# Optimization experiments

Measured on AMD Instinct MI355X. Metric: run time of the kernel, lower is better.

The kernel has to match this reference:

```python
import jax, jax.numpy as jnp
import numpy as np

B, TQ, TP, D = 4, 512, 512, 256


def setup_inputs() -> dict:
    key = jax.random.key(0)
    ks = jax.random.split(key, 5)
    return {
        "q": jax.random.normal(ks[0], (B, TQ, D), dtype=jnp.float32),
        "p": jax.random.normal(ks[1], (B, TP, D), dtype=jnp.float32),
        "W0": jax.random.normal(ks[2], (D, D), dtype=jnp.float32) / np.sqrt(D),
        "W1": jax.random.normal(ks[3], (D, D), dtype=jnp.float32) / np.sqrt(D),
        "vc": jax.random.normal(ks[4], (D, 1), dtype=jnp.float32) * 0.05,
    }


def reference(q, p, W0, W1, vc):
    # q: [B,Tq,Dq], p: [B,Tp,Dp]
    prod_q = jnp.einsum('bqd,de->bqe', q, W0)   # [B,Tq,dim]
    prod_p = jnp.einsum('bpd,de->bpe', p, W1)   # [B,Tp,dim]
    # additive attention energies: tanh over broadcast sum [B,Tp,Tq,dim]
    energy = jnp.tanh(prod_p[:, :, None, :] + prod_q[:, None, :, :])
    scores = jnp.einsum('bpqe,e->bpq', energy, vc[:, 0])  # [B,Tp,Tq]
    # original softmax is over axis=-2 of [B,Tp,Tq], i.e. the Tp axis
    weights = jax.nn.softmax(scores, axis=1)   # [B,Tp,Tq]
    # weighted sum over the Tq axis of (tiled) q
    attention_q = jnp.einsum('bpq,bqd->bpd', weights, q)  # [B,Tp,Dq]
    return attention_q
```

## Files before the change

### kernel.cpp

```cpp
#include <hip/hip_runtime.h>

#define NB 4
#define TT 512
#define DD 256
#define K2L2E    2.885390081777927f
#define NEG2L2E (-2.885390081777927f)

#if defined(__has_builtin)
# if __has_builtin(__builtin_amdgcn_global_load_lds)
#  define HAS_GLL 1
# endif
#endif

__device__ __forceinline__ void stage16(const float* __restrict__ g, float* l) {
#ifdef HAS_GLL
    __builtin_amdgcn_global_load_lds((const __attribute__((address_space(1))) void*)g,
                                     (__attribute__((address_space(3))) void*)l, 16, 0, 0);
#else
    *(float4*)l = *(const float4*)g;
#endif
}

__global__ __launch_bounds__(256) void proj_exp_kernel(
    const float* __restrict__ qin, const float* __restrict__ pin,
    const float* __restrict__ W0, const float* __restrict__ W1,
    float* __restrict__ expQ, float* __restrict__ expP)
{
    const int blk = blockIdx.x;
    const int wh = blk >> 8, tid = blk & 255;
    const int m0 = (tid >> 2) * 32, n0 = (tid & 3) * 64;
    const float* A = wh ? pin : qin;
    const float* W = wh ? W1 : W0;
    float* OUT     = wh ? expP : expQ;

    __shared__ __align__(16) float As[32 * 34];
    __shared__ __align__(16) float Bs[32 * 64];

    const int t  = threadIdx.x;
    const int ar = t >> 3, ac4 = (t & 7) * 4;
    const int br = t >> 4, bc4 = (t & 15) * 4;
    const int tn = t >> 4, tm = t & 15;

    const float* Ap = A + (long)(m0 + ar) * DD + ac4;

    float4 av  = *(const float4*)Ap;
    float4 bv0 = *(const float4*)(W + (long)br * DD + n0 + bc4);
    float4 bv1 = *(const float4*)(W + (long)(br + 16) * DD + n0 + bc4);

    float acc[2][4] = {};

    for (int c = 0; c < 8; ++c) {
        As[(ac4 + 0) * 34 + ar] = av.x;
        As[(ac4 + 1) * 34 + ar] = av.y;
        As[(ac4 + 2) * 34 + ar] = av.z;
        As[(ac4 + 3) * 34 + ar] = av.w;
        *(float4*)&Bs[br * 64 + bc4]        = bv0;
        *(float4*)&Bs[(br + 16) * 64 + bc4] = bv1;
        __syncthreads();
        if (c < 7) {
            int k1 = (c + 1) * 32;
            av  = *(const float4*)(Ap + k1);
            bv0 = *(const float4*)(W + (long)(k1 + br) * DD + n0 + bc4);
            bv1 = *(const float4*)(W + (long)(k1 + 16 + br) * DD + n0 + bc4);
        }
        #pragma unroll
        for (int kk = 0; kk < 32; ++kk) {
            float2 a = *(const float2*)&As[kk * 34 + 2 * tm];
            float4 b = *(const float4*)&Bs[kk * 64 + 4 * tn];
            float aa[2] = {a.x, a.y};
            float bb[4] = {b.x, b.y, b.z, b.w};
            #pragma unroll
            for (int i = 0; i < 2; ++i)
                #pragma unroll
                for (int j = 0; j < 4; ++j)
                    acc[i][j] = __builtin_fmaf(aa[i], bb[j], acc[i][j]);
        }
        __syncthreads();
    }

    const int  bi = m0 >> 9;
    const int  ml = (m0 & 511) + 2 * tm;
    #pragma unroll
    for (int j = 0; j < 4; ++j) {
        int d = n0 + 4 * tn + j;
        float2 st;
        st.x = __builtin_amdgcn_exp2f(acc[0][j] * K2L2E);
        st.y = __builtin_amdgcn_exp2f(acc[1][j] * K2L2E);
        *(float2*)(OUT + ((long)bi * DD + d) * TT + ml) = st;
    }
}

__global__ __launch_bounds__(512, 4) void score_kernel(
    const float* __restrict__ expP, const float* __restrict__ expQ,
    const float* __restrict__ vc, float* __restrict__ ebuf, float* __restrict__ lpart)
{
    const int b = blockIdx.z, pt = blockIdx.y, qt = blockIdx.x;
    const int p0 = pt * 32, q0 = qt * 64;
    const int t  = threadIdx.x;
    const int qx = t & 31, py = t >> 5;

    __shared__ __align__(16) float PA[2][64 * 32];
    __shared__ __align__(16) float QB[2][64 * 64];
    __shared__ float vcs[DD];

    const float* gP = expP + (long)b * DD * TT + p0;
    const float* gQ = expQ + (long)b * DD * TT + q0;

    {
        int d = t >> 3, off = (t & 7) * 4;
        stage16(gP + (long)d * TT + off, &PA[0][t * 4]);
    }
    #pragma unroll
    for (int s = 0; s < 2; ++s) {
        int f = t + 512 * s, d = f >> 4, off = (f & 15) * 4;
        stage16(gQ + (long)d * TT + off, &QB[0][f * 4]);
    }
    if (t < DD) vcs[t] = vc[t];
    __syncthreads();

    float acc[2][2] = {};

    for (int c = 0; c < 4; ++c) {
        if (c < 3) {
            int dc = (c + 1) * 64, nb = (c + 1) & 1;
            {
                int d = t >> 3, off = (t & 7) * 4;
                stage16(gP + (long)(dc + d) * TT + off, &PA[nb][t * 4]);
            }
            #pragma unroll
            for (int s = 0; s < 2; ++s) {
                int f = t + 512 * s, d = f >> 4, off = (f & 15) * 4;
                stage16(gQ + (long)(dc + d) * TT + off, &QB[nb][f * 4]);
            }
        }
        const float* PAc = PA[c & 1];
        const float* QBc = QB[c & 1];
        const float* vcb = &vcs[c * 64];
        #pragma unroll 8
        for (int dp = 0; dp < 32; ++dp) {
            float2 vp = *(const float2*)&vcb[2 * dp];
            float vs = vp.x + vp.y;
            float2 A0 = *(const float2*)&PAc[(2 * dp) * 32 + 2 * py];
            float2 A1 = *(const float2*)&PAc[(2 * dp + 1) * 32 + 2 * py];
            float2 B0 = *(const float2*)&QBc[(2 * dp) * 64 + 2 * qx];
            float2 B1 = *(const float2*)&QBc[(2 * dp + 1) * 64 + 2 * qx];
            float a0[2] = {A0.x, A0.y}, a1[2] = {A1.x, A1.y};
            float b0[2] = {B0.x, B0.y}, b1[2] = {B1.x, B1.y};
            #pragma unroll
            for (int i = 0; i < 2; ++i)
                #pragma unroll
                for (int j = 0; j < 2; ++j) {
                    float E0  = a0[i] * b0[j];
                    float E1  = a1[i] * b1[j];
                    float u   = 1.0f + (E0 + E1);
                    float den = __builtin_fmaf(E0, E1, u);
                    float num = __builtin_fmaf(vp.y, E0, __builtin_fmaf(vp.x, E1, vs));
                    acc[i][j] = __builtin_fmaf(num, __builtin_amdgcn_rcpf(den), acc[i][j]);
                }
        }
        __syncthreads();
    }

    float* eb = ebuf + ((long)b * TT + p0) * TT + q0;
    float colp[2] = {0.f, 0.f};
    #pragma unroll
    for (int i = 0; i < 2; ++i) {
        float2 ev;
        ev.x = __builtin_amdgcn_exp2f(acc[i][0] * NEG2L2E);
        ev.y = __builtin_amdgcn_exp2f(acc[i][1] * NEG2L2E);
        *(float2*)(eb + (long)(2 * py + i) * TT + 2 * qx) = ev;
        colp[0] += ev.x; colp[1] += ev.y;
    }
    float* scr = (float*)&PA[0][0];
    *(float2*)&scr[py * 64 + 2 * qx] = make_float2(colp[0], colp[1]);
    __syncthreads();
    if (t < 64) {
        float s = 0.f;
        #pragma unroll
        for (int r = 0; r < 16; ++r) s += scr[r * 64 + t];
        lpart[((long)b * 16 + pt) * TT + q0 + t] = s;
    }
}

__global__ __launch_bounds__(256) void out_kernel(
    const float* __restrict__ ebuf, const float* __restrict__ qin,
    const float* __restrict__ lpart, float* __restrict__ out)
{
    const int b = blockIdx.z, mt = blockIdx.y, nt = blockIdx.x;
    const int m0 = mt * 32, n0 = nt * 32;
    const int t  = threadIdx.x;
    const int tm = t >> 4, tn = t & 15;

    __shared__ __align__(16) float As[64 * 34];
    __shared__ __align__(16) float Bs[64 * 36];
    __shared__ float linv[TT];

    #pragma unroll
    for (int s = 0; s < 2; ++s) {
        int qq = t + 256 * s;
        float sum = 0.f;
        #pragma unroll
        for (int pb = 0; pb < 16; ++pb) sum += lpart[((long)b * 16 + pb) * TT + qq];
        linv[qq] = __builtin_amdgcn_rcpf(sum);
    }
    __syncthreads();

    const float* Ab = ebuf + ((long)b * TT + m0) * TT;
    const float* Bb = qin + (long)b * TT * DD + n0;

    const int ara = t >> 4, aca = (t & 15) * 4;
    const int brb = t >> 3, bcb = (t & 7) * 4;

    float4 av0 = *(const float4*)(Ab + (long)ara * TT + aca);
    float4 av1 = *(const float4*)(Ab + (long)(ara + 16) * TT + aca);
    float4 bv0 = *(const float4*)(Bb + (long)brb * DD + bcb);
    float4 bv1 = *(const float4*)(Bb + (long)(brb + 32) * DD + bcb);

    float acc[2][2] = {};

    for (int c = 0; c < 8; ++c) {
        const int k0 = c * 64;
        As[(aca + 0) * 34 + ara] = av0.x;
        As[(aca + 1) * 34 + ara] = av0.y;
        As[(aca + 2) * 34 + ara] = av0.z;
        As[(aca + 3) * 34 + ara] = av0.w;
        As[(aca + 0) * 34 + ara + 16] = av1.x;
        As[(aca + 1) * 34 + ara + 16] = av1.y;
        As[(aca + 2) * 34 + ara + 16] = av1.z;
        As[(aca + 3) * 34 + ara + 16] = av1.w;
        {
            float s0 = linv[k0 + brb], s1 = linv[k0 + brb + 32];
            float4 w0, w1;
            w0.x = bv0.x * s0; w0.y = bv0.y * s0; w0.z = bv0.z * s0; w0.w = bv0.w * s0;
            w1.x = bv1.x * s1; w1.y = bv1.y * s1; w1.z = bv1.z * s1; w1.w = bv1.w * s1;
            *(float4*)&Bs[brb * 36 + bcb]        = w0;
            *(float4*)&Bs[(brb + 32) * 36 + bcb] = w1;
        }
        __syncthreads();
        if (c < 7) {
            int k1 = (c + 1) * 64;
            av0 = *(const float4*)(Ab + (long)ara * TT + k1 + aca);
            av1 = *(const float4*)(Ab + (long)(ara + 16) * TT + k1 + aca);
            bv0 = *(const float4*)(Bb + (long)(k1 + brb) * DD + bcb);
            bv1 = *(const float4*)(Bb + (long)(k1 + brb + 32) * DD + bcb);
        }
        #pragma unroll
        for (int kk = 0; kk < 64; ++kk) {
            float2 a = *(const float2*)&As[kk * 34 + 2 * tm];
            float2 bb = *(const float2*)&Bs[kk * 36 + 2 * tn];
            acc[0][0] = __builtin_fmaf(a.x, bb.x, acc[0][0]);
            acc[0][1] = __builtin_fmaf(a.x, bb.y, acc[0][1]);
            acc[1][0] = __builtin_fmaf(a.y, bb.x, acc[1][0]);
            acc[1][1] = __builtin_fmaf(a.y, bb.y, acc[1][1]);
        }
        __syncthreads();
    }

    #pragma unroll
    for (int i = 0; i < 2; ++i) {
        float2 v = make_float2(acc[i][0], acc[i][1]);
        *(float2*)(out + ((long)b * TT + m0 + 2 * tm + i) * DD + n0 + 2 * tn) = v;
    }
}

extern "C" void kernel_launch(void* const* d_in, const int* in_sizes, int n_in,
                              void* d_out, int out_size, void* d_ws, size_t ws_size,
                              hipStream_t stream) {
    const float* q  = (const float*)d_in[0];
    const float* p  = (const float*)d_in[1];
    const float* W0 = (const float*)d_in[2];
    const float* W1 = (const float*)d_in[3];
    const float* vc = (const float*)d_in[4];
    float* out = (float*)d_out;

    float* ws    = (float*)d_ws;
    float* expQ  = ws;
    float* expP  = ws + 524288;
    float* ebuf  = ws + 1048576;
    float* lpart = ws + 2097152;

    proj_exp_kernel<<<dim3(512), 256, 0, stream>>>(q, p, W0, W1, expQ, expP);
    score_kernel<<<dim3(8, 16, NB), 512, 0, stream>>>(expP, expQ, vc, ebuf, lpart);
    out_kernel<<<dim3(8, 16, NB), 256, 0, stream>>>(ebuf, q, lpart, out);
}
```

Measured before the change: 128.5 us.

## Use packed FP32 FMA in score loop and retile output GEMM to 4x2

Rewrites the score kernel's inner tanh-identity math on two-wide float vectors so the compiler can emit packed FP32 instructions (v_pk_fma/v_pk_mul), roughly halving VALU issue for that hot loop. The output GEMM is retiled to 128 threads, each computing a 4x2 register tile with packed FMAs, which changes the staging pattern and the LDS padding. This raises per-thread work and register use and halves threads per block, which lowers occupancy in the out kernel.

```diff
diff --git a/kernel.cpp b/kernel.cpp
--- a/kernel.cpp
+++ b/kernel.cpp
@@ -11,6 +11,21 @@
 #  define HAS_GLL 1
 # endif
 #endif
+
+typedef float v2f __attribute__((ext_vector_type(2)));
+
+__device__ __forceinline__ v2f pk_fma(v2f a, v2f b, v2f c) {
+#if defined(__has_builtin)
+# if __has_builtin(__builtin_elementwise_fma)
+    return __builtin_elementwise_fma(a, b, c);
+# else
+    v2f r; r.x = __builtin_fmaf(a.x, b.x, c.x); r.y = __builtin_fmaf(a.y, b.y, c.y); return r;
+# endif
+#else
+    v2f r; r.x = __builtin_fmaf(a.x, b.x, c.x); r.y = __builtin_fmaf(a.y, b.y, c.y); return r;
+#endif
+}
+__device__ __forceinline__ v2f splat2(float s) { v2f r; r.x = s; r.y = s; return r; }
 
 __device__ __forceinline__ void stage16(const float* __restrict__ g, float* l) {
 #ifdef HAS_GLL
@@ -118,7 +133,7 @@
     if (t < DD) vcs[t] = vc[t];
     __syncthreads();
 
-    float acc[2][2] = {};
+    v2f acc[2]; acc[0] = splat2(0.f); acc[1] = splat2(0.f);
 
     for (int c = 0; c < 4; ++c) {
         if (c < 3) {
@@ -139,40 +154,41 @@
         #pragma unroll 8
         for (int dp = 0; dp < 32; ++dp) {
             float2 vp = *(const float2*)&vcb[2 * dp];
-            float vs = vp.x + vp.y;
+            v2f vsv = splat2(vp.x + vp.y);
+            v2f vx  = splat2(vp.x), vy = splat2(vp.y);
             float2 A0 = *(const float2*)&PAc[(2 * dp) * 32 + 2 * py];
             float2 A1 = *(const float2*)&PAc[(2 * dp + 1) * 32 + 2 * py];
-            float2 B0 = *(const float2*)&QBc[(2 * dp) * 64 + 2 * qx];
-            float2 B1 = *(const float2*)&QBc[(2 * dp + 1) * 64 + 2 * qx];
+            v2f B0 = *(const v2f*)&QBc[(2 * dp) * 64 + 2 * qx];
+            v2f B1 = *(const v2f*)&QBc[(2 * dp + 1) * 64 + 2 * qx];
             float a0[2] = {A0.x, A0.y}, a1[2] = {A1.x, A1.y};
-            float b0[2] = {B0.x, B0.y}, b1[2] = {B1.x, B1.y};
             #pragma unroll
-            for (int i = 0; i < 2; ++i)
-                #pragma unroll
-                for (int j = 0; j < 2; ++j) {
-                    float E0  = a0[i] * b0[j];
-                    float E1  = a1[i] * b1[j];
-                    float u   = 1.0f + (E0 + E1);
-                    float den = __builtin_fmaf(E0, E1, u);
-                    float num = __builtin_fmaf(vp.y, E0, __builtin_fmaf(vp.x, E1, vs));
-                    acc[i][j] = __builtin_fmaf(num, __builtin_amdgcn_rcpf(den), acc[i][j]);
-                }
+            for (int i = 0; i < 2; ++i) {
+                v2f E0  = splat2(a0[i]) * B0;
+                v2f E1  = splat2(a1[i]) * B1;
+                v2f u   = (E0 + E1) + 1.0f;
+                v2f den = pk_fma(E0, E1, u);
+                v2f num = pk_fma(vy, E0, pk_fma(vx, E1, vsv));
+                v2f r;
+                r.x = __builtin_amdgcn_rcpf(den.x);
+                r.y = __builtin_amdgcn_rcpf(den.y);
+                acc[i] = pk_fma(num, r, acc[i]);
+            }
         }
         __syncthreads();
     }
 
     float* eb = ebuf + ((long)b * TT + p0) * TT + q0;
-    float colp[2] = {0.f, 0.f};
+    v2f colp = splat2(0.f);
     #pragma unroll
     for (int i = 0; i < 2; ++i) {
         float2 ev;
-        ev.x = __builtin_amdgcn_exp2f(acc[i][0] * NEG2L2E);
-        ev.y = __builtin_amdgcn_exp2f(acc[i][1] * NEG2L2E);
+        ev.x = __builtin_amdgcn_exp2f(acc[i].x * NEG2L2E);
+        ev.y = __builtin_amdgcn_exp2f(acc[i].y * NEG2L2E);
         *(float2*)(eb + (long)(2 * py + i) * TT + 2 * qx) = ev;
-        colp[0] += ev.x; colp[1] += ev.y;
+        colp.x += ev.x; colp.y += ev.y;
     }
     float* scr = (float*)&PA[0][0];
-    *(float2*)&scr[py * 64 + 2 * qx] = make_float2(colp[0], colp[1]);
+    *(float2*)&scr[py * 64 + 2 * qx] = make_float2(colp.x, colp.y);
     __syncthreads();
     if (t < 64) {
         float s = 0.f;
@@ -182,22 +198,23 @@
     }
 }
 
-__global__ __launch_bounds__(256) void out_kernel(
+__global__ __launch_bounds__(128) void out_kernel(
     const float* __restrict__ ebuf, const float* __restrict__ qin,
     const float* __restrict__ lpart, float* __restrict__ out)
 {
-    const int b = blockIdx.z, mt = blockIdx.y, nt = blockIdx.x;
-    const int m0 = mt * 32, n0 = nt * 32;
+    const int b = blockIdx.z, pt = blockIdx.y, dt = blockIdx.x;
+    const int m0 = pt * 32, n0 = dt * 32;
     const int t  = threadIdx.x;
-    const int tm = t >> 4, tn = t & 15;
-
-    __shared__ __align__(16) float As[64 * 34];
+    const int tm = t >> 4;
+    const int tn = t & 15;
+
+    __shared__ __align__(16) float As[64 * 36];
     __shared__ __align__(16) float Bs[64 * 36];
     __shared__ float linv[TT];
 
     #pragma unroll
-    for (int s = 0; s < 2; ++s) {
-        int qq = t + 256 * s;
+    for (int s = 0; s < 4; ++s) {
+        int qq = t + 128 * s;
         float sum = 0.f;
         #pragma unroll
         for (int pb = 0; pb < 16; ++pb) sum += lpart[((long)b * 16 + pb) * TT + qq];
@@ -208,58 +225,60 @@
     const float* Ab = ebuf + ((long)b * TT + m0) * TT;
     const float* Bb = qin + (long)b * TT * DD + n0;
 
-    const int ara = t >> 4, aca = (t & 15) * 4;
-    const int brb = t >> 3, bcb = (t & 7) * 4;
-
-    float4 av0 = *(const float4*)(Ab + (long)ara * TT + aca);
-    float4 av1 = *(const float4*)(Ab + (long)(ara + 16) * TT + aca);
-    float4 bv0 = *(const float4*)(Bb + (long)brb * DD + bcb);
-    float4 bv1 = *(const float4*)(Bb + (long)(brb + 32) * DD + bcb);
-
-    float acc[2][2] = {};
+    const int ar  = t >> 2;
+    const int akc = (t & 3) * 4;
+    const int brr = t >> 3;
+    const int bc4 = (t & 7) * 4;
+
+    float4 av[4], bv[4];
+    #pragma unroll
+    for (int u = 0; u < 4; ++u) {
+        av[u] = *(const float4*)(Ab + (long)ar * TT + 16 * u + akc);
+        bv[u] = *(const float4*)(Bb + (long)(brr + 16 * u) * DD + bc4);
+    }
+
+    v2f acc[4]; acc[0] = splat2(0.f); acc[1] = splat2(0.f);
+    acc[2] = splat2(0.f); acc[3] = splat2(0.f);
 
     for (int c = 0; c < 8; ++c) {
         const int k0 = c * 64;
-        As[(aca + 0) * 34 + ara] = av0.x;
-        As[(aca + 1) * 34 + ara] = av0.y;
-        As[(aca + 2) * 34 + ara] = av0.z;
-        As[(aca + 3) * 34 + ara] = av0.w;
-        As[(aca + 0) * 34 + ara + 16] = av1.x;
-        As[(aca + 1) * 34 + ara + 16] = av1.y;
-        As[(aca + 2) * 34 + ara + 16] = av1.z;
-        As[(aca + 3) * 34 + ara + 16] = av1.w;
-        {
-            float s0 = linv[k0 + brb], s1 = linv[k0 + brb + 32];
-            float4 w0, w1;
-            w0.x = bv0.x * s0; w0.y = bv0.y * s0; w0.z = bv0.z * s0; w0.w = bv0.w * s0;
-            w1.x = bv1.x * s1; w1.y = bv1.y * s1; w1.z = bv1.z * s1; w1.w = bv1.w * s1;
-            *(float4*)&Bs[brb * 36 + bcb]        = w0;
-            *(float4*)&Bs[(brb + 32) * 36 + bcb] = w1;
+        #pragma unroll
+        for (int u = 0; u < 4; ++u) {
+            int kl = 16 * u + akc;
+            As[(kl + 0) * 36 + ar] = av[u].x;
+            As[(kl + 1) * 36 + ar] = av[u].y;
+            As[(kl + 2) * 36 + ar] = av[u].z;
+            As[(kl + 3) * 36 + ar] = av[u].w;
+            float s = linv[k0 + brr + 16 * u];
+            float4 w;
+            w.x = bv[u].x * s; w.y = bv[u].y * s; w.z = bv[u].z * s; w.w = bv[u].w * s;
+            *(float4*)&Bs[(brr + 16 * u) * 36 + bc4] = w;
         }
         __syncthreads();
         if (c < 7) {
             int k1 = (c + 1) * 64;
-            av0 = *(const float4*)(Ab + (long)ara * TT + k1 + aca);
-            av1 = *(const float4*)(Ab + (long)(ara + 16) * TT + k1 + aca);
-            bv0 = *(const float4*)(Bb + (long)(k1 + brb) * DD + bcb);
-            bv1 = *(const float4*)(Bb + (long)(k1 + brb + 32) * DD + bcb);
+            #pragma unroll
+            for (int u = 0; u < 4; ++u) {
+                av[u] = *(const float4*)(Ab + (long)ar * TT + k1 + 16 * u + akc);
+                bv[u] = *(const float4*)(Bb + (long)(k1 + brr + 16 * u) * DD + bc4);
+            }
         }
         #pragma unroll
         for (int kk = 0; kk < 64; ++kk) {
-            float2 a = *(const float2*)&As[kk * 34 + 2 * tm];
-            float2 bb = *(const float2*)&Bs[kk * 36 + 2 * tn];
-            acc[0][0] = __builtin_fmaf(a.x, bb.x, acc[0][0]);
-            acc[0][1] = __builtin_fmaf(a.x, bb.y, acc[0][1]);
-            acc[1][0] = __builtin_fmaf(a.y, bb.x, acc[1][0]);
-            acc[1][1] = __builtin_fmaf(a.y, bb.y, acc[1][1]);
-        }
-        __syncthreads();
-    }
-
-    #pragma unroll
-    for (int i = 0; i < 2; ++i) {
-        float2 v = make_float2(acc[i][0], acc[i][1]);
-        *(float2*)(out + ((long)b * TT + m0 + 2 * tm + i) * DD + n0 + 2 * tn) = v;
+            float4 a = *(const float4*)&As[kk * 36 + 4 * tm];
+            v2f bb = *(const v2f*)&Bs[kk * 36 + 2 * tn];
+            acc[0] = pk_fma(splat2(a.x), bb, acc[0]);
+            acc[1] = pk_fma(splat2(a.y), bb, acc[1]);
+            acc[2] = pk_fma(splat2(a.z), bb, acc[2]);
+            acc[3] = pk_fma(splat2(a.w), bb, acc[3]);
+        }
+        __syncthreads();
+    }
+
+    #pragma unroll
+    for (int i = 0; i < 4; ++i) {
+        *(float2*)(out + ((long)b * TT + m0 + 4 * tm + i) * DD + n0 + 2 * tn) =
+            make_float2(acc[i].x, acc[i].y);
     }
 }
 
@@ -281,5 +300,5 @@
 
     proj_exp_kernel<<<dim3(512), 256, 0, stream>>>(q, p, W0, W1, expQ, expP);
     score_kernel<<<dim3(8, 16, NB), 512, 0, stream>>>(expP, expQ, vc, ebuf, lpart);
-    out_kernel<<<dim3(8, 16, NB), 256, 0, stream>>>(ebuf, q, lpart, out);
-}
+    out_kernel<<<dim3(8, 16, NB), 128, 0, stream>>>(ebuf, q, lpart, out);
+}
```

Result: faster. 125.6 us (-2.2%).
